# Kernel optimization log

Measured on AMD Instinct MI355X. Metric: run time of the kernel, lower is better.

Reference implementation:

```python
import jax, jax.numpy as jnp
import numpy as np

B, NQ, NKV, D, H = 2, 2048, 2048, 1024, 16
DH = D // H
EPS = 1e-5


def _ln(x, g, b):
    mu = jnp.mean(x, axis=-1, keepdims=True)
    var = jnp.mean(jnp.square(x - mu), axis=-1, keepdims=True)
    return (x - mu) * jax.lax.rsqrt(var + EPS) * g + b


def setup_inputs() -> dict:
    key = jax.random.key(0)
    ks = jax.random.split(key, 16)
    s = 0.02
    return {
        "X": jax.random.normal(ks[0], (B, NQ, D), jnp.float32),
        "Y": jax.random.normal(ks[1], (B, NKV, D), jnp.float32),
        "Wq": jax.random.normal(ks[2], (D, D), jnp.float32) * s,
        "bq": jnp.zeros((D,), jnp.float32),
        "Wk": jax.random.normal(ks[3], (D, D), jnp.float32) * s,
        "bk": jnp.zeros((D,), jnp.float32),
        "Wv": jax.random.normal(ks[4], (D, D), jnp.float32) * s,
        "bv": jnp.zeros((D,), jnp.float32),
        "null_k": jax.random.normal(ks[5], (1, 1, D), jnp.float32) * s,
        "g0": jnp.ones((D,), jnp.float32),
        "b0": jnp.zeros((D,), jnp.float32),
        "g0kv": jnp.ones((D,), jnp.float32),
        "b0kv": jnp.zeros((D,), jnp.float32),
        "g1": jnp.ones((D,), jnp.float32),
        "b1": jnp.zeros((D,), jnp.float32),
        "W1": jax.random.normal(ks[6], (D, 4 * D), jnp.float32) * s,
        "bf1": jnp.zeros((4 * D,), jnp.float32),
        "W2": jax.random.normal(ks[7], (4 * D, D), jnp.float32) * s,
        "bf2": jnp.zeros((D,), jnp.float32),
    }


def reference(X, Y, Wq, bq, Wk, bk, Wv, bv, null_k, g0, b0, g0kv, b0kv,
              g1, b1, W1, bf1, W2, bf2):
    # pre-layer-norm on Q-side and KV-side inputs
    Xn = _ln(X, g0, b0)
    Yn = _ln(Y, g0kv, b0kv)
    Q = Xn @ Wq + bq                       # [B, NQ, D]
    K = Yn @ Wk + bk                       # [B, NKV, D]
    V = Yn @ Wv + bv
    # null KV: learned null key, zero value appended along seq dim
    K = jnp.concatenate([K, jnp.broadcast_to(null_k, (B, 1, D))], axis=1)   # [B, NKV+1, D]
    V = jnp.concatenate([V, jnp.zeros((B, 1, D), V.dtype)], axis=1)
    # split heads (split along feature dim == reshape to (.., H, DH))
    Qh = Q.reshape(B, NQ, H, DH)
    Kh = K.reshape(B, NKV + 1, H, DH)
    Vh = V.reshape(B, NKV + 1, H, DH)
    # scores scaled by 1/sqrt(dim_KV) (NOT head dim), softmax_temp == 1.0
    A = jnp.einsum('bqhd,bkhd->bhqk', Qh, Kh) / jnp.sqrt(jnp.float32(D))
    A = jax.nn.softmax(A, axis=-1)          # [B, H, NQ, NKV+1]
    O = jnp.einsum('bhqk,bkhd->bqhd', A, Vh).reshape(B, NQ, D)
    # no head mixing (fc_mix_heads=None); residual uses identity fc_res
    Hres = O + X
    Hr = _ln(Hres, g1, b1)
    ff = jax.nn.gelu(Hr @ W1 + bf1, approximate=False) @ W2 + bf2
    return Hres + ff
```

## Files before the change

### kernel.cpp

```cpp
#include <hip/hip_runtime.h>
#include <hip/hip_bf16.h>
#include <math.h>
#include <stdint.h>

typedef __bf16 bf16x8 __attribute__((ext_vector_type(8)));
typedef __bf16 bf16x4 __attribute__((ext_vector_type(4)));
typedef float floatx4 __attribute__((ext_vector_type(4)));
typedef short shortx4 __attribute__((ext_vector_type(4)));
typedef unsigned int uint32x2 __attribute__((ext_vector_type(2)));

#define NQS   2048
#define NKVS  2048
#define NKV1  2049
#define DM    1024
#define NH    16
#define DHD   64
#define BATCH 2
#define ROWS  (BATCH * NQS)

__device__ __forceinline__ void gld_lds16(const __bf16* gp, __bf16* lp) {
    __builtin_amdgcn_global_load_lds(
        (const __attribute__((address_space(1))) uint32_t*)(uintptr_t)gp,
        (__attribute__((address_space(3))) uint32_t*)(uintptr_t)lp,
        16, 0, 0);
}

__device__ __forceinline__ float gelu_fast(float x) {
    const float u = x * x;
    const float e = __builtin_amdgcn_exp2f(x * (-2.3022077f + (-0.1029431f) * u));
    return x * __builtin_amdgcn_rcpf(1.0f + e);
}

__global__ __launch_bounds__(256) void ln2_to_bf16(
    const float* __restrict__ X, const float* __restrict__ Y,
    const float* __restrict__ g0, const float* __restrict__ b0,
    const float* __restrict__ g0kv, const float* __restrict__ b0kv,
    __bf16* __restrict__ Xn, __bf16* __restrict__ Yn)
{
    int row = blockIdx.x;
    const float *src, *gamma, *beta; __bf16* dst;
    if (row < ROWS) { src = X; gamma = g0; beta = b0; dst = Xn; }
    else { row -= ROWS; src = Y; gamma = g0kv; beta = b0kv; dst = Yn; }
    const int tid = threadIdx.x;
    const float4 v = ((const float4*)(src + (size_t)row * DM))[tid];
    float s  = v.x + v.y + v.z + v.w;
    float sq = v.x * v.x + v.y * v.y + v.z * v.z + v.w * v.w;
    for (int off = 1; off < 64; off <<= 1) {
        s  += __shfl_xor(s, off);
        sq += __shfl_xor(sq, off);
    }
    __shared__ float red[8];
    const int wave = tid >> 6, lane = tid & 63;
    if (lane == 0) { red[wave * 2] = s; red[wave * 2 + 1] = sq; }
    __syncthreads();
    s  = red[0] + red[2] + red[4] + red[6];
    sq = red[1] + red[3] + red[5] + red[7];
    const float mu  = s * (1.0f / DM);
    const float var = sq * (1.0f / DM) - mu * mu;
    const float rs  = rsqrtf(var + 1e-5f);
    const float4 gv = ((const float4*)gamma)[tid];
    const float4 bv = ((const float4*)beta)[tid];
    bf16x4 o;
    o[0] = (__bf16)((v.x - mu) * rs * gv.x + bv.x);
    o[1] = (__bf16)((v.y - mu) * rs * gv.y + bv.y);
    o[2] = (__bf16)((v.z - mu) * rs * gv.z + bv.z);
    o[3] = (__bf16)((v.w - mu) * rs * gv.w + bv.w);
    *(bf16x4*)(dst + (size_t)row * DM + tid * 4) = o;
}

__global__ __launch_bounds__(256) void resid_ln(
    const float* __restrict__ X, const __bf16* __restrict__ O,
    const float* __restrict__ gamma, const float* __restrict__ beta,
    float* __restrict__ Hres, __bf16* __restrict__ Hr)
{
    const int row = blockIdx.x;
    const int tid = threadIdx.x;
    const float4 xv = ((const float4*)(X + (size_t)row * DM))[tid];
    const bf16x4 ov = *(const bf16x4*)(O + (size_t)row * DM + tid * 4);
    float4 v;
    v.x = xv.x + (float)ov[0];
    v.y = xv.y + (float)ov[1];
    v.z = xv.z + (float)ov[2];
    v.w = xv.w + (float)ov[3];
    ((float4*)(Hres + (size_t)row * DM))[tid] = v;

    float s  = v.x + v.y + v.z + v.w;
    float sq = v.x * v.x + v.y * v.y + v.z * v.z + v.w * v.w;
    for (int off = 1; off < 64; off <<= 1) {
        s  += __shfl_xor(s, off);
        sq += __shfl_xor(sq, off);
    }
    __shared__ float red[8];
    const int wave = tid >> 6, lane = tid & 63;
    if (lane == 0) { red[wave * 2] = s; red[wave * 2 + 1] = sq; }
    __syncthreads();
    s  = red[0] + red[2] + red[4] + red[6];
    sq = red[1] + red[3] + red[5] + red[7];
    const float mu  = s * (1.0f / DM);
    const float var = sq * (1.0f / DM) - mu * mu;
    const float rs  = rsqrtf(var + 1e-5f);
    const float4 gv = ((const float4*)gamma)[tid];
    const float4 bv = ((const float4*)beta)[tid];
    bf16x4 o;
    o[0] = (__bf16)((v.x - mu) * rs * gv.x + bv.x);
    o[1] = (__bf16)((v.y - mu) * rs * gv.y + bv.y);
    o[2] = (__bf16)((v.z - mu) * rs * gv.z + bv.z);
    o[3] = (__bf16)((v.w - mu) * rs * gv.w + bv.w);
    *(bf16x4*)(Hr + (size_t)row * DM + tid * 4) = o;
}

__global__ __launch_bounds__(256) void transpose3_f32_bf16(
    const float* __restrict__ Wq, const float* __restrict__ Wk,
    const float* __restrict__ Wv, __bf16* __restrict__ WqT,
    __bf16* __restrict__ WkT, __bf16* __restrict__ WvT)
{
    __shared__ float tile[32][33];
    const int z = blockIdx.z;
    const float* in = (z == 0) ? Wq : (z == 1) ? Wk : Wv;
    __bf16* out = (z == 0) ? WqT : (z == 1) ? WkT : WvT;
    const int c0 = blockIdx.x * 32, r0 = blockIdx.y * 32;
    const int tx = threadIdx.x, ty = threadIdx.y;
#pragma unroll
    for (int i = 0; i < 4; i++)
        tile[ty + i * 8][tx] = in[(size_t)(r0 + ty + i * 8) * DM + c0 + tx];
    __syncthreads();
#pragma unroll
    for (int i = 0; i < 4; i++)
        out[(size_t)(c0 + ty + i * 8) * DM + r0 + tx] = (__bf16)tile[tx][ty + i * 8];
}

__global__ __launch_bounds__(256) void transpose_ffw(
    const float* __restrict__ W1, const float* __restrict__ W2,
    __bf16* __restrict__ W1T, __bf16* __restrict__ W2T)
{
    __shared__ float tile[32][33];
    const int z = blockIdx.z;
    const float* in; __bf16* out; int R, C, c0, r0;
    if (z == 0) { in = W1; out = W1T; R = DM; C = 4 * DM; c0 = blockIdx.x * 32; r0 = blockIdx.y * 32; }
    else        { in = W2; out = W2T; R = 4 * DM; C = DM; c0 = blockIdx.y * 32; r0 = blockIdx.x * 32; }
    const int tx = threadIdx.x, ty = threadIdx.y;
#pragma unroll
    for (int i = 0; i < 4; i++)
        tile[ty + i * 8][tx] = in[(size_t)(r0 + ty + i * 8) * C + c0 + tx];
    __syncthreads();
#pragma unroll
    for (int i = 0; i < 4; i++)
        out[(size_t)(c0 + ty + i * 8) * R + r0 + tx] = (__bf16)tile[tx][ty + i * 8];
}

__global__ __launch_bounds__(256) void fill_null(
    const float* __restrict__ null_k, __bf16* __restrict__ Kb,
    __bf16* __restrict__ Vt)
{
    const int i = blockIdx.x * 256 + threadIdx.x;
    if (i < BATCH * DM) {
        const int b = i >> 10, d = i & (DM - 1);
        Kb[((size_t)b * NKV1 + NKVS) * DM + d] = (__bf16)null_k[d];
    }
    if (i < BATCH * NH * DHD * 8) {
        const int bhd = i >> 3, kvp = i & 7;
        Vt[(size_t)bhd * 2056 + 2048 + kvp] = (__bf16)0.0f;
    }
}

__device__ __forceinline__ void g256_loop(
    const __bf16* __restrict__ A, const __bf16* __restrict__ Bt,
    int Kst, int kbeg, int m0, int n0,
    __bf16* sa, __bf16* sb, floatx4 (&acc)[8][4])
{
    const int tid = threadIdx.x, lane = tid & 63;
    const int g = lane >> 4, c = lane & 15;
    const int wave = tid >> 6;
    const int wm = wave >> 2, wn = wave & 3;

    const int r = tid >> 2, j = tid & 3;
    const int jx = (j ^ (r & 3)) * 8;
    const __bf16* Ag = A  + (size_t)(m0 + r) * Kst + kbeg + jx;
    const __bf16* Bg = Bt + (size_t)(n0 + r) * Kst + kbeg + jx;
    __bf16* la = sa + tid * 8;
    __bf16* lb = sb + tid * 8;

#define G256_STAGE(ss, koff) do {                                          \
    gld_lds16(Ag + (koff),                      la + (ss) * 8192);         \
    gld_lds16(Ag + (size_t)128 * Kst + (koff),  la + (ss) * 8192 + 4096);  \
    gld_lds16(Bg + (koff),                      lb + (ss) * 8192);         \
    gld_lds16(Bg + (size_t)128 * Kst + (koff),  lb + (ss) * 8192 + 4096);  \
} while (0)

    G256_STAGE(0, 0);
    G256_STAGE(1, 32);
    G256_STAGE(2, 64);

    const int ca = (c & 3) * 8;
    const __bf16* ra = sa + (wm * 128 + c) * 32;
    const __bf16* rb = sb + (wn * 64 + c) * 32;

    for (int s = 0; s < 32; s++) {
        if (s < 29) {
            G256_STAGE((s + 3) & 3, (s + 3) * 32);
            asm volatile("s_waitcnt vmcnt(12)" ::: "memory");
        } else if (s == 29) {
            asm volatile("s_waitcnt vmcnt(8)" ::: "memory");
        } else if (s == 30) {
            asm volatile("s_waitcnt vmcnt(4)" ::: "memory");
        } else {
            asm volatile("s_waitcnt vmcnt(0)" ::: "memory");
        }
        __builtin_amdgcn_sched_barrier(0);
        __builtin_amdgcn_s_barrier();
        asm volatile("" ::: "memory");

        const int ss = (s & 3) * 8192;
        bf16x8 af[8], bfr[4];
#pragma unroll
        for (int i = 0; i < 8; i++)
            af[i] = *(const bf16x8*)(ra + ss + i * 512 + ((g * 8) ^ ca));
#pragma unroll
        for (int jj = 0; jj < 4; jj++)
            bfr[jj] = *(const bf16x8*)(rb + ss + jj * 512 + ((g * 8) ^ ca));

        __builtin_amdgcn_s_setprio(1);
#pragma unroll
        for (int i = 0; i < 8; i++)
#pragma unroll
            for (int jj = 0; jj < 4; jj++)
                acc[i][jj] = __builtin_amdgcn_mfma_f32_16x16x32_bf16(
                    af[i], bfr[jj], acc[i][jj], 0, 0, 0);
        __builtin_amdgcn_s_setprio(0);
        __builtin_amdgcn_sched_barrier(0);
        __builtin_amdgcn_s_barrier();
        asm volatile("" ::: "memory");
    }
#undef G256_STAGE
}

template<int NX>
__device__ __forceinline__ void g256_decode(int bid, int ntot, int& m0, int& n0)
{
    const int cpx = ntot >> 3;
    const int l = (bid & 7) * cpx + (bid >> 3);
    m0 = (l / NX) * 256;
    n0 = (l % NX) * 256;
}

template<int MODE, int ACT, int NX>
__global__ __launch_bounds__(512, 2) void g256(
    const __bf16* __restrict__ A, const __bf16* __restrict__ Bt,
    const float* __restrict__ bias, void* __restrict__ outp,
    int M, int N, int Kst)
{
    __shared__ __bf16 SA[4][256][32];
    __shared__ __bf16 SB[4][256][32];
    int m0, n0;
    g256_decode<NX>(blockIdx.x, NX * (M >> 8), m0, n0);
    const int kbeg = (MODE == 4) ? (blockIdx.z << 10) : 0;

    floatx4 acc[8][4] = {};
    g256_loop(A, Bt, Kst, kbeg, m0, n0, &SA[0][0][0], &SB[0][0][0], acc);

    const int tid = threadIdx.x, lane = tid & 63, wave = tid >> 6;
    const int g = lane >> 4, c = lane & 15;
    const int wm = wave >> 2, wn = wave & 3;

    __bf16* obf = (__bf16*)outp;
    float*  of  = (float*)outp;
#pragma unroll
    for (int i = 0; i < 8; i++) {
#pragma unroll
        for (int jj = 0; jj < 4; jj++) {
            const int row = m0 + wm * 128 + i * 16 + g * 4;
            const int col = n0 + wn * 64 + jj * 16 + c;
            const float bb = (MODE == 4) ? 0.0f : bias[col];
            float xs[4];
#pragma unroll
            for (int rr = 0; rr < 4; rr++) {
                float x = acc[i][jj][rr] + bb;
                if (ACT == 1) x = gelu_fast(x);
                xs[rr] = x;
            }
            if (MODE == 0) {
#pragma unroll
                for (int rr = 0; rr < 4; rr++)
                    obf[(size_t)(row + rr) * N + col] = (__bf16)xs[rr];
            } else if (MODE == 4) {
#pragma unroll
                for (int rr = 0; rr < 4; rr++)
                    of[((size_t)blockIdx.z * M + row + rr) * N + col] = xs[rr];
            }
        }
    }
}

__global__ __launch_bounds__(512, 2) void g256qkv(
    const __bf16* __restrict__ Xn, const __bf16* __restrict__ Yn,
    const __bf16* __restrict__ WqT, const __bf16* __restrict__ WkT,
    const __bf16* __restrict__ WvT,
    const float* __restrict__ bq, const float* __restrict__ bk,
    const float* __restrict__ bv,
    __bf16* __restrict__ Qbf, __bf16* __restrict__ Kbf,
    __bf16* __restrict__ Vt)
{
    __shared__ __bf16 SA[4][256][32];
    __shared__ __bf16 SB[4][256][32];
    const int z = blockIdx.z;
    const __bf16* A    = (z == 0) ? Xn  : Yn;
    const __bf16* Bt   = (z == 0) ? WqT : (z == 1) ? WkT : WvT;
    const float*  bias = (z == 0) ? bq  : (z == 1) ? bk  : bv;

    int m0, n0;
    g256_decode<4>(blockIdx.x, 64, m0, n0);

    floatx4 acc[8][4] = {};
    g256_loop(A, Bt, DM, 0, m0, n0, &SA[0][0][0], &SB[0][0][0], acc);

    const int tid = threadIdx.x, lane = tid & 63, wave = tid >> 6;
    const int g = lane >> 4, c = lane & 15;
    const int wm = wave >> 2, wn = wave & 3;

#pragma unroll
    for (int i = 0; i < 8; i++) {
#pragma unroll
        for (int jj = 0; jj < 4; jj++) {
            const int row = m0 + wm * 128 + i * 16 + g * 4;
            const int col = n0 + wn * 64 + jj * 16 + c;
            const float bb = bias[col];
            float xs[4];
#pragma unroll
            for (int rr = 0; rr < 4; rr++) xs[rr] = acc[i][jj][rr] + bb;
            if (z == 0) {
#pragma unroll
                for (int rr = 0; rr < 4; rr++)
                    Qbf[(size_t)(row + rr) * DM + col] = (__bf16)xs[rr];
            } else if (z == 1) {
#pragma unroll
                for (int rr = 0; rr < 4; rr++) {
                    const int r2 = row + rr;
                    Kbf[(size_t)(r2 + (r2 >> 11)) * DM + col] = (__bf16)xs[rr];
                }
            } else {
                const int b  = row >> 11;
                const int kv = row & 2047;
                const size_t base =
                    ((size_t)((b * NH + (col >> 6)) * DHD + (col & 63))) * 2056 + kv;
                bf16x4 pk;
                pk[0] = (__bf16)xs[0]; pk[1] = (__bf16)xs[1];
                pk[2] = (__bf16)xs[2]; pk[3] = (__bf16)xs[3];
                *(bf16x4*)(Vt + base) = pk;
            }
        }
    }
}

__global__ __launch_bounds__(256) void ff2_reduce(
    const float* __restrict__ part, const float* __restrict__ bias,
    const float* __restrict__ Hres, float* __restrict__ out)
{
    const size_t f4 = (size_t)blockIdx.x * 256 + threadIdx.x;
    const int c4 = (int)(f4 & (DM / 4 - 1));
    const size_t stride4 = (size_t)ROWS * DM / 4;
    float4 a = ((const float4*)part)[f4];
    const float4 p1 = ((const float4*)part)[f4 + stride4];
    const float4 p2 = ((const float4*)part)[f4 + 2 * stride4];
    const float4 p3 = ((const float4*)part)[f4 + 3 * stride4];
    const float4 b  = ((const float4*)bias)[c4];
    const float4 hr = ((const float4*)Hres)[f4];
    a.x += p1.x + p2.x + p3.x + b.x + hr.x;
    a.y += p1.y + p2.y + p3.y + b.y + hr.y;
    a.z += p1.z + p2.z + p3.z + b.z + hr.z;
    a.w += p1.w + p2.w + p3.w + b.w + hr.w;
    ((float4*)out)[f4] = a;
}

__global__ __launch_bounds__(256, 2) void attn_kernel(
    const __bf16* __restrict__ Q, const __bf16* __restrict__ Kb,
    const __bf16* __restrict__ Vt, __bf16* __restrict__ O)
{
    __shared__ __bf16 Ks[2][64][64];
    __shared__ __bf16 Vs[2][64][64];

    const int tid = threadIdx.x, lane = tid & 63, w = tid >> 6;
    const int g = lane >> 4, c = lane & 15;

    const int hw   = blockIdx.x;
    const int slot = hw >> 3;
    const int hb   = (hw & 7) | ((slot >> 4) << 3);
    const int h = hb & 15, b = hb >> 4;
    const int q0w = (slot & 15) * 128 + w * 32;

    const float QSC = 0.03125f * 1.44269504088896f;
    bf16x8 qf[2][2];
#pragma unroll
    for (int qt = 0; qt < 2; qt++) {
        const __bf16* Qbase = Q + ((size_t)(b * NQS + q0w + qt * 16 + c)) * DM + h * DHD;
        qf[qt][0] = *(const bf16x8*)(Qbase + g * 8);
        qf[qt][1] = *(const bf16x8*)(Qbase + 32 + g * 8);
#pragma unroll
        for (int e = 0; e < 8; e++) {
            qf[qt][0][e] = (__bf16)((float)qf[qt][0][e] * QSC);
            qf[qt][1][e] = (__bf16)((float)qf[qt][1][e] * QSC);
        }
    }

    floatx4 lacc[2] = {};
    floatx4 oacc[2][4] = {};

    const int srow = tid >> 3;
    const int schk = (tid & 7) ^ (srow & 7);
    const __bf16* Kg  = Kb + (size_t)b * NKV1 * DM + h * DHD + schk * 8;
    const __bf16* Vg  = Vt + ((size_t)(b * NH + h) * DHD + srow) * 2056;
    const __bf16* Vg2 = Vg + (size_t)32 * 2056;
    const int vcol0 = schk * 8;

    auto stage = [&](int p, int kv0, bool tail) {
        __bf16* kd0 = &Ks[p][0][0]  + tid * 8;
        __bf16* kd1 = &Ks[p][32][0] + tid * 8;
        __bf16* vd0 = &Vs[p][0][0]  + tid * 8;
        __bf16* vd1 = &Vs[p][32][0] + tid * 8;
        if (!tail) {
            gld_lds16(Kg + (size_t)(kv0 + srow) * DM, kd0);
            gld_lds16(Kg + (size_t)(kv0 + srow + 32) * DM, kd1);
            gld_lds16(Vg + kv0 + vcol0, vd0);
            gld_lds16(Vg2 + kv0 + vcol0, vd1);
        } else {
            const int r0 = min(kv0 + srow, NKVS);
            const int r1 = min(kv0 + srow + 32, NKVS);
            const int vc = min(kv0 + vcol0, NKVS);
            gld_lds16(Kg + (size_t)r0 * DM, kd0);
            gld_lds16(Kg + (size_t)r1 * DM, kd1);
            gld_lds16(Vg + vc, vd0);
            gld_lds16(Vg2 + vc, vd1);
        }
    };

    auto compute = [&](int p, int kv0, bool tail) {
        floatx4 s[2][4];
#pragma unroll
        for (int qt = 0; qt < 2; qt++)
#pragma unroll
            for (int kvt = 0; kvt < 4; kvt++)
#pragma unroll
                for (int r = 0; r < 4; r++) s[qt][kvt][r] = -6.0f;

        const int sw = c & 7;
        __builtin_amdgcn_s_setprio(1);
#pragma unroll
        for (int kvt = 0; kvt < 4; kvt++) {
            const bf16x8 kf0 = *(const bf16x8*)&Ks[p][kvt * 16 + c][(g ^ sw) * 8];
            const bf16x8 kf1 = *(const bf16x8*)&Ks[p][kvt * 16 + c][((4 | g) ^ sw) * 8];
#pragma unroll
            for (int qt = 0; qt < 2; qt++) {
                s[qt][kvt] = __builtin_amdgcn_mfma_f32_16x16x32_bf16(kf0, qf[qt][0], s[qt][kvt], 0, 0, 0);
                s[qt][kvt] = __builtin_amdgcn_mfma_f32_16x16x32_bf16(kf1, qf[qt][1], s[qt][kvt], 0, 0, 0);
            }
        }
        __builtin_amdgcn_s_setprio(0);

        if (tail) {
#pragma unroll
            for (int qt = 0; qt < 2; qt++)
#pragma unroll
                for (int kvt = 0; kvt < 4; kvt++)
#pragma unroll
                    for (int r = 0; r < 4; r++)
                        if (kv0 + kvt * 16 + g * 4 + r >= NKV1) s[qt][kvt][r] = -1e30f;
        }

        shortx4 pf[2][4];
#pragma unroll
        for (int qt = 0; qt < 2; qt++)
#pragma unroll
            for (int kvt = 0; kvt < 4; kvt++) {
                float p0 = __builtin_amdgcn_exp2f(s[qt][kvt][0]);
                float p1 = __builtin_amdgcn_exp2f(s[qt][kvt][1]);
                float p2 = __builtin_amdgcn_exp2f(s[qt][kvt][2]);
                float p3 = __builtin_amdgcn_exp2f(s[qt][kvt][3]);
                lacc[qt][0] += p0; lacc[qt][1] += p1;
                lacc[qt][2] += p2; lacc[qt][3] += p3;
                uint32x2 pk;
                pk[0] = (__builtin_bit_cast(unsigned int, p0) >> 16) |
                        (__builtin_bit_cast(unsigned int, p1) & 0xFFFF0000u);
                pk[1] = (__builtin_bit_cast(unsigned int, p2) >> 16) |
                        (__builtin_bit_cast(unsigned int, p3) & 0xFFFF0000u);
                pf[qt][kvt] = __builtin_bit_cast(shortx4, pk);
            }

        __builtin_amdgcn_s_setprio(1);
#pragma unroll
        for (int kvt = 0; kvt < 4; kvt++) {
            shortx4 vfr[4];
#pragma unroll
            for (int dt = 0; dt < 4; dt++) {
                const int slotp = (kvt * 2 + (g >> 1)) ^ sw;
                vfr[dt] = *(const shortx4*)&Vs[p][dt * 16 + c][slotp * 8 + (g & 1) * 4];
            }
#pragma unroll
            for (int dt = 0; dt < 4; dt++)
#pragma unroll
                for (int qt = 0; qt < 2; qt++)
                    oacc[qt][dt] = __builtin_amdgcn_mfma_f32_16x16x16bf16_1k(
                        vfr[dt], pf[qt][kvt], oacc[qt][dt], 0, 0, 0);
        }
        __builtin_amdgcn_s_setprio(0);
    };

    stage(0, 0, false);
    __syncthreads();
    for (int it = 0; it < 32; it++) {
        stage((it + 1) & 1, (it + 1) * 64, it == 31);
        compute(it & 1, it * 64, false);
        __syncthreads();
    }
    compute(0, 2048, true);

#pragma unroll
    for (int qt = 0; qt < 2; qt++) {
        float l = lacc[qt][0] + lacc[qt][1] + lacc[qt][2] + lacc[qt][3];
        l += __shfl_xor(l, 16);
        l += __shfl_xor(l, 32);
        const float inv_l = 1.0f / l;
        __bf16* Ob = O + ((size_t)(b * NQS + q0w + qt * 16 + c)) * DM + h * DHD;
#pragma unroll
        for (int dt = 0; dt < 4; dt++) {
            bf16x4 ob;
#pragma unroll
            for (int r = 0; r < 4; r++) ob[r] = (__bf16)(oacc[qt][dt][r] * inv_l);
            *(bf16x4*)(Ob + dt * 16 + g * 4) = ob;
        }
    }
}

extern "C" void kernel_launch(void* const* d_in, const int* in_sizes, int n_in,
                              void* d_out, int out_size, void* d_ws, size_t ws_size,
                              hipStream_t stream)
{
    const float* X      = (const float*)d_in[0];
    const float* Y      = (const float*)d_in[1];
    const float* Wq     = (const float*)d_in[2];
    const float* bq     = (const float*)d_in[3];
    const float* Wk     = (const float*)d_in[4];
    const float* bk     = (const float*)d_in[5];
    const float* Wv     = (const float*)d_in[6];
    const float* bv     = (const float*)d_in[7];
    const float* null_k = (const float*)d_in[8];
    const float* g0     = (const float*)d_in[9];
    const float* b0     = (const float*)d_in[10];
    const float* g0kv   = (const float*)d_in[11];
    const float* b0kv   = (const float*)d_in[12];
    const float* g1     = (const float*)d_in[13];
    const float* b1     = (const float*)d_in[14];
    const float* W1     = (const float*)d_in[15];
    const float* bf1    = (const float*)d_in[16];
    const float* W2     = (const float*)d_in[17];
    const float* bf2    = (const float*)d_in[18];
    float* out = (float*)d_out;

    char* p = (char*)d_ws;
    __bf16* W2T  = (__bf16*)p; p += (size_t)4 * DM * DM * 2;
    float*  Hres = (float*)p;  p += (size_t)ROWS * DM * 4;
    __bf16* Gbf  = (__bf16*)p; p += (size_t)ROWS * 4 * DM * 2;
    char* scratch = p;
    __bf16* Xn   = (__bf16*)p; p += (size_t)ROWS * DM * 2;
    __bf16* Yn   = (__bf16*)p; p += (size_t)ROWS * DM * 2;
    __bf16* WqT  = (__bf16*)p; p += (size_t)DM * DM * 2;
    __bf16* WkT  = (__bf16*)p; p += (size_t)DM * DM * 2;
    __bf16* WvT  = (__bf16*)p; p += (size_t)DM * DM * 2;
    __bf16* W1T  = (__bf16*)p; p += (size_t)4 * DM * DM * 2;
    __bf16* Qbf  = (__bf16*)p; p += (size_t)ROWS * DM * 2;
    __bf16* Kbf  = (__bf16*)p; p += (size_t)BATCH * NKV1 * DM * 2;
    __bf16* Vt   = (__bf16*)p; p += (size_t)BATCH * NH * DHD * 2056 * 2;
    __bf16* Obf  = (__bf16*)p; p += (size_t)ROWS * DM * 2;
    __bf16* Hr   = (__bf16*)p; p += (size_t)ROWS * DM * 2;
    float* Part  = (float*)scratch;

    ln2_to_bf16<<<2 * ROWS, 256, 0, stream>>>(X, Y, g0, b0, g0kv, b0kv, Xn, Yn);

    transpose3_f32_bf16<<<dim3(DM / 32, DM / 32, 3), dim3(32, 8), 0, stream>>>(
        Wq, Wk, Wv, WqT, WkT, WvT);
    transpose_ffw<<<dim3(128, 32, 2), dim3(32, 8), 0, stream>>>(W1, W2, W1T, W2T);

    g256qkv<<<dim3(64, 1, 3), 512, 0, stream>>>(
        Xn, Yn, WqT, WkT, WvT, bq, bk, bv, Qbf, Kbf, Vt);
    fill_null<<<64, 256, 0, stream>>>(null_k, Kbf, Vt);

    attn_kernel<<<dim3(512), 256, 0, stream>>>(Qbf, Kbf, Vt, Obf);

    resid_ln<<<ROWS, 256, 0, stream>>>(X, Obf, g1, b1, Hres, Hr);

    g256<0, 1, 16><<<dim3(256), 512, 0, stream>>>(
        Hr, W1T, bf1, (void*)Gbf, ROWS, 4 * DM, DM);
    g256<4, 0, 4><<<dim3(64, 1, 4), 512, 0, stream>>>(
        Gbf, W2T, bf2, (void*)Part, ROWS, DM, 4 * DM);
    ff2_reduce<<<ROWS * DM / 1024, 256, 0, stream>>>(Part, bf2, Hres, out);
}
```

Before: 349.1 us.

## Fuse split-K FF2 reduction into atomics and compute softmax denominator via MFMA

The residual+LN kernel now writes Hres+bf2 directly into the output, and the split-K FF2 GEMM accumulates its four partial results into the output with float atomicAdd. This removes the separate reduce kernel and the fp32 partial buffers. The attention kernel computes the softmax row sum with an extra MFMA against a vector of ones instead of per-lane adds and cross-lane shuffles, and uses v_perm to pack bf16 values. The trade-offs are atomic traffic with non-deterministic summation order, and the row sum is now taken over bf16-rounded probabilities.

```diff
diff --git a/kernel.cpp b/kernel.cpp
--- a/kernel.cpp
+++ b/kernel.cpp
@@ -7,7 +7,6 @@
 typedef __bf16 bf16x4 __attribute__((ext_vector_type(4)));
 typedef float floatx4 __attribute__((ext_vector_type(4)));
 typedef short shortx4 __attribute__((ext_vector_type(4)));
-typedef unsigned int uint32x2 __attribute__((ext_vector_type(2)));
 
 #define NQS   2048
 #define NKVS  2048
@@ -71,7 +70,8 @@
 __global__ __launch_bounds__(256) void resid_ln(
     const float* __restrict__ X, const __bf16* __restrict__ O,
     const float* __restrict__ gamma, const float* __restrict__ beta,
-    float* __restrict__ Hres, __bf16* __restrict__ Hr)
+    const float* __restrict__ bf2, float* __restrict__ out,
+    __bf16* __restrict__ Hr)
 {
     const int row = blockIdx.x;
     const int tid = threadIdx.x;
@@ -82,7 +82,11 @@
     v.y = xv.y + (float)ov[1];
     v.z = xv.z + (float)ov[2];
     v.w = xv.w + (float)ov[3];
-    ((float4*)(Hres + (size_t)row * DM))[tid] = v;
+    const float4 b2 = ((const float4*)bf2)[tid];
+    float4 o0;
+    o0.x = v.x + b2.x; o0.y = v.y + b2.y;
+    o0.z = v.z + b2.z; o0.w = v.w + b2.w;
+    ((float4*)(out + (size_t)row * DM))[tid] = o0;
 
     float s  = v.x + v.y + v.z + v.w;
     float sq = v.x * v.x + v.y * v.y + v.z * v.z + v.w * v.w;
@@ -253,7 +257,7 @@
     __shared__ __bf16 SB[4][256][32];
     int m0, n0;
     g256_decode<NX>(blockIdx.x, NX * (M >> 8), m0, n0);
-    const int kbeg = (MODE == 4) ? (blockIdx.z << 10) : 0;
+    const int kbeg = (MODE == 5) ? (blockIdx.z << 10) : 0;
 
     floatx4 acc[8][4] = {};
     g256_loop(A, Bt, Kst, kbeg, m0, n0, &SA[0][0][0], &SB[0][0][0], acc);
@@ -270,7 +274,7 @@
         for (int jj = 0; jj < 4; jj++) {
             const int row = m0 + wm * 128 + i * 16 + g * 4;
             const int col = n0 + wn * 64 + jj * 16 + c;
-            const float bb = (MODE == 4) ? 0.0f : bias[col];
+            const float bb = (MODE == 5) ? 0.0f : bias[col];
             float xs[4];
 #pragma unroll
             for (int rr = 0; rr < 4; rr++) {
@@ -282,10 +286,10 @@
 #pragma unroll
                 for (int rr = 0; rr < 4; rr++)
                     obf[(size_t)(row + rr) * N + col] = (__bf16)xs[rr];
-            } else if (MODE == 4) {
+            } else if (MODE == 5) {
 #pragma unroll
                 for (int rr = 0; rr < 4; rr++)
-                    of[((size_t)blockIdx.z * M + row + rr) * N + col] = xs[rr];
+                    atomicAdd(&of[(size_t)(row + rr) * N + col], xs[rr]);
             }
         }
     }
@@ -351,26 +355,6 @@
     }
 }
 
-__global__ __launch_bounds__(256) void ff2_reduce(
-    const float* __restrict__ part, const float* __restrict__ bias,
-    const float* __restrict__ Hres, float* __restrict__ out)
-{
-    const size_t f4 = (size_t)blockIdx.x * 256 + threadIdx.x;
-    const int c4 = (int)(f4 & (DM / 4 - 1));
-    const size_t stride4 = (size_t)ROWS * DM / 4;
-    float4 a = ((const float4*)part)[f4];
-    const float4 p1 = ((const float4*)part)[f4 + stride4];
-    const float4 p2 = ((const float4*)part)[f4 + 2 * stride4];
-    const float4 p3 = ((const float4*)part)[f4 + 3 * stride4];
-    const float4 b  = ((const float4*)bias)[c4];
-    const float4 hr = ((const float4*)Hres)[f4];
-    a.x += p1.x + p2.x + p3.x + b.x + hr.x;
-    a.y += p1.y + p2.y + p3.y + b.y + hr.y;
-    a.z += p1.z + p2.z + p3.z + b.z + hr.z;
-    a.w += p1.w + p2.w + p3.w + b.w + hr.w;
-    ((float4*)out)[f4] = a;
-}
-
 __global__ __launch_bounds__(256, 2) void attn_kernel(
     const __bf16* __restrict__ Q, const __bf16* __restrict__ Kb,
     const __bf16* __restrict__ Vt, __bf16* __restrict__ O)
@@ -401,7 +385,10 @@
         }
     }
 
-    floatx4 lacc[2] = {};
+    shortx4 ones;
+    ones[0] = ones[1] = ones[2] = ones[3] = (short)0x3F80;
+
+    floatx4 dacc[2] = {};
     floatx4 oacc[2][4] = {};
 
     const int srow = tid >> 3;
@@ -470,17 +457,13 @@
         for (int qt = 0; qt < 2; qt++)
 #pragma unroll
             for (int kvt = 0; kvt < 4; kvt++) {
-                float p0 = __builtin_amdgcn_exp2f(s[qt][kvt][0]);
-                float p1 = __builtin_amdgcn_exp2f(s[qt][kvt][1]);
-                float p2 = __builtin_amdgcn_exp2f(s[qt][kvt][2]);
-                float p3 = __builtin_amdgcn_exp2f(s[qt][kvt][3]);
-                lacc[qt][0] += p0; lacc[qt][1] += p1;
-                lacc[qt][2] += p2; lacc[qt][3] += p3;
-                uint32x2 pk;
-                pk[0] = (__builtin_bit_cast(unsigned int, p0) >> 16) |
-                        (__builtin_bit_cast(unsigned int, p1) & 0xFFFF0000u);
-                pk[1] = (__builtin_bit_cast(unsigned int, p2) >> 16) |
-                        (__builtin_bit_cast(unsigned int, p3) & 0xFFFF0000u);
+                const unsigned u0 = __builtin_bit_cast(unsigned, __builtin_amdgcn_exp2f(s[qt][kvt][0]));
+                const unsigned u1 = __builtin_bit_cast(unsigned, __builtin_amdgcn_exp2f(s[qt][kvt][1]));
+                const unsigned u2 = __builtin_bit_cast(unsigned, __builtin_amdgcn_exp2f(s[qt][kvt][2]));
+                const unsigned u3 = __builtin_bit_cast(unsigned, __builtin_amdgcn_exp2f(s[qt][kvt][3]));
+                unsigned pk0 = __builtin_amdgcn_perm(u1, u0, 0x07060302u);
+                unsigned pk1 = __builtin_amdgcn_perm(u3, u2, 0x07060302u);
+                unsigned long long pk = ((unsigned long long)pk1 << 32) | pk0;
                 pf[qt][kvt] = __builtin_bit_cast(shortx4, pk);
             }
 
@@ -499,6 +482,10 @@
                 for (int qt = 0; qt < 2; qt++)
                     oacc[qt][dt] = __builtin_amdgcn_mfma_f32_16x16x16bf16_1k(
                         vfr[dt], pf[qt][kvt], oacc[qt][dt], 0, 0, 0);
+#pragma unroll
+            for (int qt = 0; qt < 2; qt++)
+                dacc[qt] = __builtin_amdgcn_mfma_f32_16x16x16bf16_1k(
+                    ones, pf[qt][kvt], dacc[qt], 0, 0, 0);
         }
         __builtin_amdgcn_s_setprio(0);
     };
@@ -514,10 +501,7 @@
 
 #pragma unroll
     for (int qt = 0; qt < 2; qt++) {
-        float l = lacc[qt][0] + lacc[qt][1] + lacc[qt][2] + lacc[qt][3];
-        l += __shfl_xor(l, 16);
-        l += __shfl_xor(l, 32);
-        const float inv_l = 1.0f / l;
+        const float inv_l = 1.0f / dacc[qt][0];
         __bf16* Ob = O + ((size_t)(b * NQS + q0w + qt * 16 + c)) * DM + h * DHD;
 #pragma unroll
         for (int dt = 0; dt < 4; dt++) {
@@ -556,9 +540,7 @@
 
     char* p = (char*)d_ws;
     __bf16* W2T  = (__bf16*)p; p += (size_t)4 * DM * DM * 2;
-    float*  Hres = (float*)p;  p += (size_t)ROWS * DM * 4;
     __bf16* Gbf  = (__bf16*)p; p += (size_t)ROWS * 4 * DM * 2;
-    char* scratch = p;
     __bf16* Xn   = (__bf16*)p; p += (size_t)ROWS * DM * 2;
     __bf16* Yn   = (__bf16*)p; p += (size_t)ROWS * DM * 2;
     __bf16* WqT  = (__bf16*)p; p += (size_t)DM * DM * 2;
@@ -570,7 +552,6 @@
     __bf16* Vt   = (__bf16*)p; p += (size_t)BATCH * NH * DHD * 2056 * 2;
     __bf16* Obf  = (__bf16*)p; p += (size_t)ROWS * DM * 2;
     __bf16* Hr   = (__bf16*)p; p += (size_t)ROWS * DM * 2;
-    float* Part  = (float*)scratch;
 
     ln2_to_bf16<<<2 * ROWS, 256, 0, stream>>>(X, Y, g0, b0, g0kv, b0kv, Xn, Yn);
 
@@ -584,11 +565,10 @@
 
     attn_kernel<<<dim3(512), 256, 0, stream>>>(Qbf, Kbf, Vt, Obf);
 
-    resid_ln<<<ROWS, 256, 0, stream>>>(X, Obf, g1, b1, Hres, Hr);
+    resid_ln<<<ROWS, 256, 0, stream>>>(X, Obf, g1, b1, bf2, out, Hr);
 
     g256<0, 1, 16><<<dim3(256), 512, 0, stream>>>(
         Hr, W1T, bf1, (void*)Gbf, ROWS, 4 * DM, DM);
-    g256<4, 0, 4><<<dim3(64, 1, 4), 512, 0, stream>>>(
-        Gbf, W2T, bf2, (void*)Part, ROWS, DM, 4 * DM);
-    ff2_reduce<<<ROWS * DM / 1024, 256, 0, stream>>>(Part, bf2, Hres, out);
-}
+    g256<5, 0, 4><<<dim3(64, 1, 4), 512, 0, stream>>>(
+        Gbf, W2T, nullptr, (void*)out, ROWS, DM, 4 * DM);
+}
```

Result: slower. 376.5 us (+7.8%).

## Quad-buffer KV tiles, compute softmax denominator via MFMA, pack probabilities with perm

Applied to the files above, without the earlier changes.

The attention kernel moves from double to quad LDS buffering and processes two KV tiles per barrier, which halves the number of __syncthreads in the main loop. The softmax row sum is now taken by an extra MFMA against a vector of bf16 ones instead of VALU adds plus shuffles. The fp32-to-bf16 packing uses v_perm, and the denominator is now summed from the rounded bf16 probabilities, which matches what the PV product uses. The cost is doubled LDS per block (64KB), which may limit occupancy to two blocks per CU, and the added MFMA work.

```diff
diff --git a/kernel.cpp b/kernel.cpp
--- a/kernel.cpp
+++ b/kernel.cpp
@@ -7,7 +7,6 @@
 typedef __bf16 bf16x4 __attribute__((ext_vector_type(4)));
 typedef float floatx4 __attribute__((ext_vector_type(4)));
 typedef short shortx4 __attribute__((ext_vector_type(4)));
-typedef unsigned int uint32x2 __attribute__((ext_vector_type(2)));
 
 #define NQS   2048
 #define NKVS  2048
@@ -375,8 +374,8 @@
     const __bf16* __restrict__ Q, const __bf16* __restrict__ Kb,
     const __bf16* __restrict__ Vt, __bf16* __restrict__ O)
 {
-    __shared__ __bf16 Ks[2][64][64];
-    __shared__ __bf16 Vs[2][64][64];
+    __shared__ __bf16 Ks[4][64][64];
+    __shared__ __bf16 Vs[4][64][64];
 
     const int tid = threadIdx.x, lane = tid & 63, w = tid >> 6;
     const int g = lane >> 4, c = lane & 15;
@@ -401,7 +400,10 @@
         }
     }
 
-    floatx4 lacc[2] = {};
+    shortx4 ones;
+    ones[0] = ones[1] = ones[2] = ones[3] = (short)0x3F80;
+
+    floatx4 dacc[2] = {};
     floatx4 oacc[2][4] = {};
 
     const int srow = tid >> 3;
@@ -470,17 +472,13 @@
         for (int qt = 0; qt < 2; qt++)
 #pragma unroll
             for (int kvt = 0; kvt < 4; kvt++) {
-                float p0 = __builtin_amdgcn_exp2f(s[qt][kvt][0]);
-                float p1 = __builtin_amdgcn_exp2f(s[qt][kvt][1]);
-                float p2 = __builtin_amdgcn_exp2f(s[qt][kvt][2]);
-                float p3 = __builtin_amdgcn_exp2f(s[qt][kvt][3]);
-                lacc[qt][0] += p0; lacc[qt][1] += p1;
-                lacc[qt][2] += p2; lacc[qt][3] += p3;
-                uint32x2 pk;
-                pk[0] = (__builtin_bit_cast(unsigned int, p0) >> 16) |
-                        (__builtin_bit_cast(unsigned int, p1) & 0xFFFF0000u);
-                pk[1] = (__builtin_bit_cast(unsigned int, p2) >> 16) |
-                        (__builtin_bit_cast(unsigned int, p3) & 0xFFFF0000u);
+                const unsigned u0 = __builtin_bit_cast(unsigned, __builtin_amdgcn_exp2f(s[qt][kvt][0]));
+                const unsigned u1 = __builtin_bit_cast(unsigned, __builtin_amdgcn_exp2f(s[qt][kvt][1]));
+                const unsigned u2 = __builtin_bit_cast(unsigned, __builtin_amdgcn_exp2f(s[qt][kvt][2]));
+                const unsigned u3 = __builtin_bit_cast(unsigned, __builtin_amdgcn_exp2f(s[qt][kvt][3]));
+                unsigned pk0 = __builtin_amdgcn_perm(u1, u0, 0x07060302u);
+                unsigned pk1 = __builtin_amdgcn_perm(u3, u2, 0x07060302u);
+                unsigned long long pk = ((unsigned long long)pk1 << 32) | pk0;
                 pf[qt][kvt] = __builtin_bit_cast(shortx4, pk);
             }
 
@@ -499,25 +497,29 @@
                 for (int qt = 0; qt < 2; qt++)
                     oacc[qt][dt] = __builtin_amdgcn_mfma_f32_16x16x16bf16_1k(
                         vfr[dt], pf[qt][kvt], oacc[qt][dt], 0, 0, 0);
+#pragma unroll
+            for (int qt = 0; qt < 2; qt++)
+                dacc[qt] = __builtin_amdgcn_mfma_f32_16x16x16bf16_1k(
+                    ones, pf[qt][kvt], dacc[qt], 0, 0, 0);
         }
         __builtin_amdgcn_s_setprio(0);
     };
 
     stage(0, 0, false);
+    stage(1, 64, false);
     __syncthreads();
-    for (int it = 0; it < 32; it++) {
-        stage((it + 1) & 1, (it + 1) * 64, it == 31);
-        compute(it & 1, it * 64, false);
+    for (int it = 0; it < 32; it += 2) {
+        stage((it + 2) & 3, (it + 2) * 64, (it + 2) == 32);
+        if (it + 3 <= 32) stage((it + 3) & 3, (it + 3) * 64, false);
+        compute(it & 3, it * 64, false);
+        compute((it + 1) & 3, (it + 1) * 64, false);
         __syncthreads();
     }
     compute(0, 2048, true);
 
 #pragma unroll
     for (int qt = 0; qt < 2; qt++) {
-        float l = lacc[qt][0] + lacc[qt][1] + lacc[qt][2] + lacc[qt][3];
-        l += __shfl_xor(l, 16);
-        l += __shfl_xor(l, 32);
-        const float inv_l = 1.0f / l;
+        const float inv_l = 1.0f / dacc[qt][0];
         __bf16* Ob = O + ((size_t)(b * NQS + q0w + qt * 16 + c)) * DM + h * DHD;
 #pragma unroll
         for (int dt = 0; dt < 4; dt++) {
```

New measurement: 353.0 us. No clear change (+1.1%).
